# Optimization experiments

Measured on AMD Instinct MI355X. Metric: run time of the kernel, lower is better.

The kernel has to match this reference:

```python
import jax, jax.numpy as jnp
import numpy as np

D_MODEL = 1024
N_HEADS = 16
D_K = D_MODEL // N_HEADS
B, S = 2, 2048


def setup_inputs() -> dict:
    key = jax.random.key(0)
    ks = jax.random.split(key, 11)
    s = 1.0 / np.sqrt(D_MODEL)
    return {
        "q": jax.random.normal(ks[0], (B, S, D_MODEL), jnp.float32),
        "k": jax.random.normal(ks[1], (B, S, D_MODEL), jnp.float32),
        "v": jax.random.normal(ks[2], (B, S, D_MODEL), jnp.float32),
        "Wq": jax.random.normal(ks[3], (D_MODEL, D_MODEL), jnp.float32) * s,
        "bq": jnp.zeros((D_MODEL,), jnp.float32),
        "Wk": jax.random.normal(ks[4], (D_MODEL, D_MODEL), jnp.float32) * s,
        "bk": jnp.zeros((D_MODEL,), jnp.float32),
        "Wv": jax.random.normal(ks[5], (D_MODEL, D_MODEL), jnp.float32) * s,
        "bv": jnp.zeros((D_MODEL,), jnp.float32),
        "Wo": jax.random.normal(ks[6], (D_MODEL, D_MODEL), jnp.float32) * s,
        "bo": jnp.zeros((D_MODEL,), jnp.float32),
    }


def reference(q, k, v, Wq, bq, Wk, bk, Wv, bv, Wo, bo):
    b = q.shape[0]
    # linear projections then split heads: [b, s, d] -> [b, h, s, d_k]
    def proj(x, W, bias):
        y = jnp.einsum('bsd,ed->bse', x, W) + bias  # torch Linear: x @ W.T + b
        return y.reshape(b, -1, N_HEADS, D_K).transpose(0, 2, 1, 3)

    qh, kh, vh = proj(q, Wq, bq), proj(k, Wk, bk), proj(v, Wv, bv)
    scores = jnp.einsum('bhqd,bhkd->bhqk', qh, kh) / np.sqrt(D_K)
    attn = jax.nn.softmax(scores, axis=-1)  # dropout: identity (eval mode)
    x = jnp.einsum('bhqk,bhkd->bhqd', attn, vh)
    x = x.transpose(0, 2, 1, 3).reshape(b, -1, D_MODEL)
    return jnp.einsum('bsd,ed->bse', x, Wo) + bo
```

## Files before the change

kernel.cpp:

```cpp
#include <hip/hip_runtime.h>
#include <math.h>
#include <stdint.h>

#define DM 1024
#define NH 16
#define DKH 64
#define BB 2
#define SS 2048
#define MM (BB*SS)

typedef __bf16 bf16;
typedef __bf16 bf16x8 __attribute__((ext_vector_type(8)));
typedef float f32x4 __attribute__((ext_vector_type(4)));

#define MFMA16(a,b,c) __builtin_amdgcn_mfma_f32_16x16x32_bf16((a),(b),(c),0,0,0)

#define SOFTMAX_C 12.0f
#define QSCALE 0.1803368801111204f

__device__ static inline void g2l16(const void* g, void* l) {
  __builtin_amdgcn_global_load_lds(
      (const __attribute__((address_space(1))) unsigned int*)g,
      (__attribute__((address_space(3))) unsigned int*)l, 16, 0, 0);
}

__global__ __launch_bounds__(256) void cvt_all(
    const float* __restrict__ q, const float* __restrict__ k, const float* __restrict__ v,
    const float* __restrict__ wq, const float* __restrict__ wk,
    const float* __restrict__ wv, const float* __restrict__ wo,
    bf16* __restrict__ Xq, bf16* __restrict__ Xk, bf16* __restrict__ Xv,
    bf16* __restrict__ Wqb, bf16* __restrict__ Wkb, bf16* __restrict__ Wvb,
    bf16* __restrict__ Wob)
{
  const long i = (long)blockIdx.x * 256 + threadIdx.x;
  const float* src; bf16* dst; long off;
  if (i < 3L * 524288L) {
    const int a = (int)(i / 524288L);
    off = (i % 524288L) * 8;
    src = (a == 0) ? q : (a == 1) ? k : v;
    dst = (a == 0) ? Xq : (a == 1) ? Xk : Xv;
  } else {
    const long j = i - 3L * 524288L;
    const int a = (int)(j / 131072L);
    off = (j % 131072L) * 8;
    src = (a == 0) ? wq : (a == 1) ? wk : (a == 2) ? wv : wo;
    dst = (a == 0) ? Wqb : (a == 1) ? Wkb : (a == 2) ? Wvb : Wob;
  }
  float4 f0 = *(const float4*)(src + off);
  float4 f1 = *(const float4*)(src + off + 4);
  bf16x8 o;
  o[0] = (bf16)f0.x; o[1] = (bf16)f0.y; o[2] = (bf16)f0.z; o[3] = (bf16)f0.w;
  o[4] = (bf16)f1.x; o[5] = (bf16)f1.y; o[6] = (bf16)f1.z; o[7] = (bf16)f1.w;
  *(bf16x8*)(dst + off) = o;
}

template<int EP, int BN>
__device__ __forceinline__ void gemm_bt_body(
    const bf16* __restrict__ A, const bf16* __restrict__ W,
    const float* __restrict__ bias, void* __restrict__ Y, float scale)
{
  constexpr int NT = BN / 32;
  constexpr int PB = BN / 32;
  __shared__ __align__(16) char smem[16384 + BN * 128];
  const int tid = threadIdx.x;
  const int lane = tid & 63, w = tid >> 6;
  const int ln15 = lane & 15, q4 = lane >> 4;
  const int m0 = blockIdx.x * 128;
  const int n0 = blockIdx.y * BN;
  const int mhalf = (w >> 1) * 64, nhalf = (w & 1) * (BN / 2);

  const bf16* gA[4]; const bf16* gB[PB];
  char* lA[4]; char* lB[PB];
  #pragma unroll
  for (int p = 0; p < 4; ++p) {
    const int n = p * 256 + tid;
    const int row = n >> 3, u = n & 7;
    const int g = u ^ (row & 7);
    gA[p] = A + (size_t)(m0 + row) * DM + g * 8;
    lA[p] = smem + n * 16;
  }
  #pragma unroll
  for (int p = 0; p < PB; ++p) {
    const int n = p * 256 + tid;
    const int row = n >> 3, u = n & 7;
    const int g = u ^ (row & 7);
    gB[p] = W + (size_t)(n0 + row) * DM + g * 8;
    lB[p] = smem + 16384 + n * 16;
  }

  int aoff[4][2], boff[NT][2];
  #pragma unroll
  for (int mt = 0; mt < 4; ++mt) {
    const int row = mhalf + mt * 16 + ln15;
    #pragma unroll
    for (int kc = 0; kc < 2; ++kc)
      aoff[mt][kc] = (row * 8 + ((kc * 4 + q4) ^ (row & 7))) * 16;
  }
  #pragma unroll
  for (int nt = 0; nt < NT; ++nt) {
    const int row = nhalf + nt * 16 + ln15;
    #pragma unroll
    for (int kc = 0; kc < 2; ++kc)
      boff[nt][kc] = 16384 + (row * 8 + ((kc * 4 + q4) ^ (row & 7))) * 16;
  }

  f32x4 acc[4][NT] = {};

  for (int kt = 0; kt < DM; kt += 64) {
    __syncthreads();
    #pragma unroll
    for (int p = 0; p < 4; ++p) g2l16(gA[p] + kt, lA[p]);
    #pragma unroll
    for (int p = 0; p < PB; ++p) g2l16(gB[p] + kt, lB[p]);
    asm volatile("s_waitcnt vmcnt(0)" ::: "memory");
    __syncthreads();
    #pragma unroll
    for (int kc = 0; kc < 2; ++kc) {
      bf16x8 af[4];
      #pragma unroll
      for (int mt = 0; mt < 4; ++mt) af[mt] = *(const bf16x8*)(smem + aoff[mt][kc]);
      #pragma unroll
      for (int nt = 0; nt < NT; ++nt) {
        bf16x8 bfr = *(const bf16x8*)(smem + boff[nt][kc]);
        #pragma unroll
        for (int mt = 0; mt < 4; ++mt)
          acc[mt][nt] = MFMA16(af[mt], bfr, acc[mt][nt]);
      }
    }
  }

  #pragma unroll
  for (int nt = 0; nt < NT; ++nt) {
    const int col = n0 + nhalf + nt * 16 + ln15;
    const float bv = bias[col];
    #pragma unroll
    for (int mt = 0; mt < 4; ++mt) {
      #pragma unroll
      for (int r = 0; r < 4; ++r) {
        const int row = m0 + mhalf + mt * 16 + q4 * 4 + r;
        const float val = (acc[mt][nt][r] + bv) * scale;
        if (EP == 0) {
          ((float*)Y)[(size_t)row * DM + col] = val;
        } else {
          const int b = row >> 11, s = row & 2047;
          const int h = col >> 6, dk = col & 63;
          ((bf16*)Y)[(((size_t)(b * NH + h) * SS + s) * DKH) + dk] = (bf16)val;
        }
      }
    }
  }
}

__global__ __launch_bounds__(256) void gemm_qkv(
    const bf16* Xq, const bf16* Xk, const bf16* Xv,
    const bf16* Wq, const bf16* Wk, const bf16* Wv,
    const float* bq, const float* bk, const float* bv,
    bf16* qh, bf16* kh, bf16* vh)
{
  const int z = blockIdx.z;
  const bf16* A = (z == 0) ? Xq : (z == 1) ? Xk : Xv;
  const bf16* W = (z == 0) ? Wq : (z == 1) ? Wk : Wv;
  const float* bias = (z == 0) ? bq : (z == 1) ? bk : bv;
  bf16* Y = (z == 0) ? qh : (z == 1) ? kh : vh;
  const float scale = (z == 0) ? QSCALE : 1.0f;
  gemm_bt_body<1, 128>(A, W, bias, Y, scale);
}

__global__ __launch_bounds__(256) void gemm_out(
    const bf16* A, const bf16* W, const float* bias, float* Y)
{
  gemm_bt_body<0, 64>(A, W, bias, Y, 1.0f);
}

__global__ __launch_bounds__(256) void transpose_v(
    const bf16* __restrict__ vh, bf16* __restrict__ vth)
{
  __shared__ unsigned short Ls[64][66];
  const int bh = blockIdx.y;
  const int s0 = blockIdx.x * 64;
  const int tid = threadIdx.x;
  const unsigned short* src = (const unsigned short*)(vh + (size_t)bh * SS * DKH);
  unsigned short* dst = (unsigned short*)(vth + (size_t)bh * SS * DKH);
  #pragma unroll
  for (int p = 0; p < 2; ++p) {
    const int n = p * 256 + tid;
    const int sl = n >> 3, dc = (n & 7) * 8;
    uint4 a = *(const uint4*)(src + (size_t)(s0 + sl) * DKH + dc);
    Ls[sl][dc + 0] = (unsigned short)(a.x & 0xffff);
    Ls[sl][dc + 1] = (unsigned short)(a.x >> 16);
    Ls[sl][dc + 2] = (unsigned short)(a.y & 0xffff);
    Ls[sl][dc + 3] = (unsigned short)(a.y >> 16);
    Ls[sl][dc + 4] = (unsigned short)(a.z & 0xffff);
    Ls[sl][dc + 5] = (unsigned short)(a.z >> 16);
    Ls[sl][dc + 6] = (unsigned short)(a.w & 0xffff);
    Ls[sl][dc + 7] = (unsigned short)(a.w >> 16);
  }
  __syncthreads();
  #pragma unroll
  for (int p = 0; p < 2; ++p) {
    const int n = p * 256 + tid;
    const int dk = n >> 3, sc = (n & 7) * 8;
    uint4 o;
    o.x = (unsigned)Ls[sc + 0][dk] | ((unsigned)Ls[sc + 1][dk] << 16);
    o.y = (unsigned)Ls[sc + 2][dk] | ((unsigned)Ls[sc + 3][dk] << 16);
    o.z = (unsigned)Ls[sc + 4][dk] | ((unsigned)Ls[sc + 5][dk] << 16);
    o.w = (unsigned)Ls[sc + 6][dk] | ((unsigned)Ls[sc + 7][dk] << 16);
    *(uint4*)(dst + (size_t)dk * SS + s0 + sc) = o;
  }
}

__global__ __launch_bounds__(256) void attn_mfma(
    const bf16* __restrict__ Qh, const bf16* __restrict__ Kh,
    const bf16* __restrict__ Vth, bf16* __restrict__ Xout)
{
  __shared__ __align__(16) char smem[51200];
  const int tid = threadIdx.x, lane = tid & 63, w = tid >> 6;
  const int ln15 = lane & 15, q4 = lane >> 4;
  const int bh = blockIdx.y, b = bh >> 4, h = bh & 15;
  const int q0 = blockIdx.x * 128 + w * 32;
  const bf16* Qb = Qh + (size_t)bh * SS * DKH;
  const bf16* Kb = Kh + (size_t)bh * SS * DKH;
  const bf16* Vb = Vth + (size_t)bh * SS * DKH;

  bf16x8 qf[2][2];
  #pragma unroll
  for (int mt = 0; mt < 2; ++mt)
    #pragma unroll
    for (int kc = 0; kc < 2; ++kc)
      qf[mt][kc] = *(const bf16x8*)(Qb + (size_t)(q0 + mt * 16 + ln15) * DKH + kc * 32 + q4 * 8);

  bf16x8 ones_frag;
  {
    const bf16 o = (ln15 == 0) ? (bf16)1.0f : (bf16)0.0f;
    #pragma unroll
    for (int j = 0; j < 8; ++j) ones_frag[j] = o;
  }

  const bf16* gK[2]; const bf16* gV[2];
  char* lK[2]; char* lV[2];
  #pragma unroll
  for (int p = 0; p < 2; ++p) {
    const int n = p * 256 + tid;
    const int row = n >> 3, u = n & 7;
    const int g = u ^ (row & 7);
    gK[p] = Kb + (size_t)row * DKH + g * 8;
    gV[p] = Vb + (size_t)row * SS + g * 8;
    lK[p] = smem + n * 16;
    lV[p] = smem + 8192 + n * 16;
  }
  char* Pl = smem + 32768 + w * 4608;

  int koff[4][2], voff[4][2], poff[2][2];
  #pragma unroll
  for (int nt = 0; nt < 4; ++nt) {
    const int rowi = nt * 16 + ln15;
    #pragma unroll
    for (int kc = 0; kc < 2; ++kc) {
      koff[nt][kc] = (rowi * 8 + ((kc * 4 + q4) ^ (rowi & 7))) * 16;
      voff[nt][kc] = 8192 + (rowi * 8 + ((kc * 4 + q4) ^ (rowi & 7))) * 16;
    }
  }
  #pragma unroll
  for (int mt = 0; mt < 2; ++mt)
    #pragma unroll
    for (int kc = 0; kc < 2; ++kc)
      poff[mt][kc] = ((mt * 16 + ln15) * 9 + kc * 4 + q4) * 16;

  f32x4 Oa[2][4] = {};
  f32x4 Ol[2] = {};

  #pragma unroll
  for (int p = 0; p < 2; ++p) {
    g2l16(gK[p], lK[p]); g2l16(gV[p], lV[p]);
    gK[p] += 64 * DKH; gV[p] += 64;
  }

  for (int kt = 0; kt < SS / 64; ++kt) {
    const int cur = (kt & 1) << 14;
    asm volatile("s_waitcnt vmcnt(0)" ::: "memory");
    __syncthreads();
    if (kt < SS / 64 - 1) {
      const int nxt = (~kt & 1) << 14;
      #pragma unroll
      for (int p = 0; p < 2; ++p) {
        g2l16(gK[p], lK[p] + nxt); g2l16(gV[p], lV[p] + nxt);
        gK[p] += 64 * DKH; gV[p] += 64;
      }
    }

    f32x4 S[2][4];
    #pragma unroll
    for (int mt = 0; mt < 2; ++mt)
      #pragma unroll
      for (int nt = 0; nt < 4; ++nt)
        S[mt][nt] = (f32x4){-SOFTMAX_C, -SOFTMAX_C, -SOFTMAX_C, -SOFTMAX_C};
    #pragma unroll
    for (int kc = 0; kc < 2; ++kc) {
      #pragma unroll
      for (int nt = 0; nt < 4; ++nt) {
        bf16x8 kf = *(const bf16x8*)(smem + cur + koff[nt][kc]);
        #pragma unroll
        for (int mt = 0; mt < 2; ++mt)
          S[mt][nt] = MFMA16(qf[mt][kc], kf, S[mt][nt]);
      }
    }

    #pragma unroll
    for (int mt = 0; mt < 2; ++mt)
      #pragma unroll
      for (int nt = 0; nt < 4; ++nt)
        #pragma unroll
        for (int r = 0; r < 4; ++r) {
          const int prow = mt * 16 + q4 * 4 + r;
          const int key = nt * 16 + ln15;
          *(bf16*)(Pl + prow * 144 + key * 2) =
              (bf16)__builtin_amdgcn_exp2f(S[mt][nt][r]);
        }
    asm volatile("s_waitcnt lgkmcnt(0)" ::: "memory");

    #pragma unroll
    for (int kc = 0; kc < 2; ++kc) {
      bf16x8 pf[2];
      #pragma unroll
      for (int mt = 0; mt < 2; ++mt) pf[mt] = *(const bf16x8*)(Pl + poff[mt][kc]);
      #pragma unroll
      for (int nt = 0; nt < 4; ++nt) {
        bf16x8 vf = *(const bf16x8*)(smem + cur + voff[nt][kc]);
        #pragma unroll
        for (int mt = 0; mt < 2; ++mt)
          Oa[mt][nt] = MFMA16(pf[mt], vf, Oa[mt][nt]);
      }
      #pragma unroll
      for (int mt = 0; mt < 2; ++mt)
        Ol[mt] = MFMA16(pf[mt], ones_frag, Ol[mt]);
    }
  }

  #pragma unroll
  for (int mt = 0; mt < 2; ++mt)
    #pragma unroll
    for (int r = 0; r < 4; ++r) {
      const float l = __shfl(Ol[mt][r], lane & 48);
      const float inv = 1.f / l;
      const int srow = q0 + mt * 16 + q4 * 4 + r;
      #pragma unroll
      for (int nt = 0; nt < 4; ++nt) {
        const int col = h * DKH + nt * 16 + ln15;
        Xout[((size_t)(b * SS + srow)) * DM + col] = (bf16)(Oa[mt][nt][r] * inv);
      }
    }
}

extern "C" void kernel_launch(void* const* d_in, const int* in_sizes, int n_in,
                              void* d_out, int out_size, void* d_ws, size_t ws_size,
                              hipStream_t stream)
{
  const float* q  = (const float*)d_in[0];
  const float* k  = (const float*)d_in[1];
  const float* v  = (const float*)d_in[2];
  const float* Wq = (const float*)d_in[3];
  const float* bq = (const float*)d_in[4];
  const float* Wk = (const float*)d_in[5];
  const float* bk = (const float*)d_in[6];
  const float* Wv = (const float*)d_in[7];
  const float* bv = (const float*)d_in[8];
  const float* Wo = (const float*)d_in[9];
  const float* bo = (const float*)d_in[10];
  float* out = (float*)d_out;

  char* ws = (char*)d_ws;
  const size_t MB = 1u << 20;
  bf16* Xq  = (bf16*)(ws + 0);
  bf16* Xk  = (bf16*)(ws + 8 * MB);
  bf16* Xv  = (bf16*)(ws + 16 * MB);
  bf16* Wqb = (bf16*)(ws + 24 * MB);
  bf16* Wkb = (bf16*)(ws + 26 * MB);
  bf16* Wvb = (bf16*)(ws + 28 * MB);
  bf16* Wob = (bf16*)(ws + 30 * MB);
  bf16* qh  = (bf16*)(ws + 32 * MB);
  bf16* kh  = (bf16*)(ws + 40 * MB);
  bf16* vh  = (bf16*)(ws + 48 * MB);
  bf16* vth = (bf16*)(ws + 56 * MB);
  bf16* xh  = Xq;

  cvt_all<<<8192, 256, 0, stream>>>(q, k, v, Wq, Wk, Wv, Wo,
                                    Xq, Xk, Xv, Wqb, Wkb, Wvb, Wob);

  gemm_qkv<<<dim3(32, 8, 3), 256, 0, stream>>>(Xq, Xk, Xv, Wqb, Wkb, Wvb,
                                               bq, bk, bv, qh, kh, vh);

  transpose_v<<<dim3(32, 32), 256, 0, stream>>>(vh, vth);

  attn_mfma<<<dim3(16, 32), 256, 0, stream>>>(qh, kh, vth, xh);

  gemm_out<<<dim3(32, 16), 256, 0, stream>>>(xh, Wob, bo, out);
}
```

Baseline: 225.3 us.

## Keep attention probabilities in registers via transposed QK^T and K16 MFMA

Computes S transposed (K as the A operand) so each lane's exp'd scores already form the A-operand layout of a 16x16x16 bf16 MFMA. P can then feed the PV product directly from registers instead of round-tripping through LDS. The row sum moves from an extra MFMA against a ones fragment to register adds plus cross-lane shuffles. This cuts LDS use from 51200 to 32768 bytes, which may raise occupancy, and adjusts the V LDS offsets for 4-element fragments. The K16 MFMA issues twice as many instructions per unit of work as the K32 one.

```diff
diff --git a/kernel.cpp b/kernel.cpp
--- a/kernel.cpp
+++ b/kernel.cpp
@@ -11,9 +11,21 @@
 
 typedef __bf16 bf16;
 typedef __bf16 bf16x8 __attribute__((ext_vector_type(8)));
+typedef __bf16 bf16x4 __attribute__((ext_vector_type(4)));
+typedef short s16x4 __attribute__((ext_vector_type(4)));
 typedef float f32x4 __attribute__((ext_vector_type(4)));
 
 #define MFMA16(a,b,c) __builtin_amdgcn_mfma_f32_16x16x32_bf16((a),(b),(c),0,0,0)
+
+#if __has_builtin(__builtin_amdgcn_mfma_f32_16x16x16bf16_1k)
+#define MFMAK16(a,b,c) __builtin_amdgcn_mfma_f32_16x16x16bf16_1k((a),(b),(c),0,0,0)
+#else
+__device__ static inline f32x4 mfma_k16_asm(s16x4 a, s16x4 b, f32x4 c) {
+  asm("v_mfma_f32_16x16x16_bf16 %0, %1, %2, %0" : "+v"(c) : "v"(a), "v"(b));
+  return c;
+}
+#define MFMAK16(a,b,c) mfma_k16_asm((a),(b),(c))
+#endif
 
 #define SOFTMAX_C 12.0f
 #define QSCALE 0.1803368801111204f
@@ -213,7 +225,7 @@
     const bf16* __restrict__ Qh, const bf16* __restrict__ Kh,
     const bf16* __restrict__ Vth, bf16* __restrict__ Xout)
 {
-  __shared__ __align__(16) char smem[51200];
+  __shared__ __align__(16) char smem[32768];
   const int tid = threadIdx.x, lane = tid & 63, w = tid >> 6;
   const int ln15 = lane & 15, q4 = lane >> 4;
   const int bh = blockIdx.y, b = bh >> 4, h = bh & 15;
@@ -229,13 +241,6 @@
     for (int kc = 0; kc < 2; ++kc)
       qf[mt][kc] = *(const bf16x8*)(Qb + (size_t)(q0 + mt * 16 + ln15) * DKH + kc * 32 + q4 * 8);
 
-  bf16x8 ones_frag;
-  {
-    const bf16 o = (ln15 == 0) ? (bf16)1.0f : (bf16)0.0f;
-    #pragma unroll
-    for (int j = 0; j < 8; ++j) ones_frag[j] = o;
-  }
-
   const bf16* gK[2]; const bf16* gV[2];
   char* lK[2]; char* lV[2];
   #pragma unroll
@@ -248,26 +253,20 @@
     lK[p] = smem + n * 16;
     lV[p] = smem + 8192 + n * 16;
   }
-  char* Pl = smem + 32768 + w * 4608;
-
-  int koff[4][2], voff[4][2], poff[2][2];
-  #pragma unroll
-  for (int nt = 0; nt < 4; ++nt) {
-    const int rowi = nt * 16 + ln15;
-    #pragma unroll
-    for (int kc = 0; kc < 2; ++kc) {
-      koff[nt][kc] = (rowi * 8 + ((kc * 4 + q4) ^ (rowi & 7))) * 16;
-      voff[nt][kc] = 8192 + (rowi * 8 + ((kc * 4 + q4) ^ (rowi & 7))) * 16;
-    }
-  }
-  #pragma unroll
-  for (int mt = 0; mt < 2; ++mt)
-    #pragma unroll
-    for (int kc = 0; kc < 2; ++kc)
-      poff[mt][kc] = ((mt * 16 + ln15) * 9 + kc * 4 + q4) * 16;
+
+  int koff[2];
+  #pragma unroll
+  for (int kc = 0; kc < 2; ++kc)
+    koff[kc] = (ln15 * 8 + ((kc * 4 + q4) ^ (ln15 & 7))) * 16;
+  int voff[4];
+  #pragma unroll
+  for (int dt = 0; dt < 4; ++dt) {
+    const int row = dt * 16 + ln15;
+    voff[dt] = 8192 + row * 128 + (((q4 >> 1) ^ (row & 7)) * 16) + (q4 & 1) * 8;
+  }
 
   f32x4 Oa[2][4] = {};
-  f32x4 Ol[2] = {};
+  float lsum[2] = {0.f, 0.f};
 
   #pragma unroll
   for (int p = 0; p < 2; ++p) {
@@ -288,67 +287,68 @@
       }
     }
 
-    f32x4 S[2][4];
-    #pragma unroll
-    for (int mt = 0; mt < 2; ++mt)
-      #pragma unroll
-      for (int nt = 0; nt < 4; ++nt)
-        S[mt][nt] = (f32x4){-SOFTMAX_C, -SOFTMAX_C, -SOFTMAX_C, -SOFTMAX_C};
+    f32x4 S[4][2];
+    #pragma unroll
+    for (int nt = 0; nt < 4; ++nt)
+      #pragma unroll
+      for (int mt = 0; mt < 2; ++mt)
+        S[nt][mt] = (f32x4){-SOFTMAX_C, -SOFTMAX_C, -SOFTMAX_C, -SOFTMAX_C};
     #pragma unroll
     for (int kc = 0; kc < 2; ++kc) {
       #pragma unroll
       for (int nt = 0; nt < 4; ++nt) {
-        bf16x8 kf = *(const bf16x8*)(smem + cur + koff[nt][kc]);
+        const bf16x8 kf = *(const bf16x8*)(smem + cur + koff[kc] + nt * 2048);
         #pragma unroll
         for (int mt = 0; mt < 2; ++mt)
-          S[mt][nt] = MFMA16(qf[mt][kc], kf, S[mt][nt]);
-      }
-    }
-
-    #pragma unroll
-    for (int mt = 0; mt < 2; ++mt)
-      #pragma unroll
-      for (int nt = 0; nt < 4; ++nt)
-        #pragma unroll
-        for (int r = 0; r < 4; ++r) {
-          const int prow = mt * 16 + q4 * 4 + r;
-          const int key = nt * 16 + ln15;
-          *(bf16*)(Pl + prow * 144 + key * 2) =
-              (bf16)__builtin_amdgcn_exp2f(S[mt][nt][r]);
-        }
-    asm volatile("s_waitcnt lgkmcnt(0)" ::: "memory");
-
-    #pragma unroll
-    for (int kc = 0; kc < 2; ++kc) {
-      bf16x8 pf[2];
-      #pragma unroll
-      for (int mt = 0; mt < 2; ++mt) pf[mt] = *(const bf16x8*)(Pl + poff[mt][kc]);
+          S[nt][mt] = MFMA16(kf, qf[mt][kc], S[nt][mt]);
+      }
+    }
+
+    s16x4 pf[2][4];
+    #pragma unroll
+    for (int mt = 0; mt < 2; ++mt) {
       #pragma unroll
       for (int nt = 0; nt < 4; ++nt) {
-        bf16x8 vf = *(const bf16x8*)(smem + cur + voff[nt][kc]);
+        const float p0 = __builtin_amdgcn_exp2f(S[nt][mt][0]);
+        const float p1 = __builtin_amdgcn_exp2f(S[nt][mt][1]);
+        const float p2 = __builtin_amdgcn_exp2f(S[nt][mt][2]);
+        const float p3 = __builtin_amdgcn_exp2f(S[nt][mt][3]);
+        lsum[mt] += (p0 + p1) + (p2 + p3);
+        union { bf16x4 b; s16x4 s; } u;
+        u.b[0] = (bf16)p0; u.b[1] = (bf16)p1; u.b[2] = (bf16)p2; u.b[3] = (bf16)p3;
+        pf[mt][nt] = u.s;
+      }
+    }
+
+    #pragma unroll
+    for (int nt = 0; nt < 4; ++nt) {
+      #pragma unroll
+      for (int dt = 0; dt < 4; ++dt) {
+        const s16x4 vf = *(const s16x4*)(smem + cur + (voff[dt] ^ (nt << 5)));
         #pragma unroll
         for (int mt = 0; mt < 2; ++mt)
-          Oa[mt][nt] = MFMA16(pf[mt], vf, Oa[mt][nt]);
-      }
-      #pragma unroll
-      for (int mt = 0; mt < 2; ++mt)
-        Ol[mt] = MFMA16(pf[mt], ones_frag, Ol[mt]);
-    }
-  }
-
-  #pragma unroll
-  for (int mt = 0; mt < 2; ++mt)
+          Oa[mt][dt] = MFMAK16(pf[mt][nt], vf, Oa[mt][dt]);
+      }
+    }
+  }
+
+  #pragma unroll
+  for (int mt = 0; mt < 2; ++mt) {
+    float l = lsum[mt];
+    l += __shfl_xor(l, 16);
+    l += __shfl_xor(l, 32);
     #pragma unroll
     for (int r = 0; r < 4; ++r) {
-      const float l = __shfl(Ol[mt][r], lane & 48);
-      const float inv = 1.f / l;
+      const float lr = __shfl(l, (q4 << 2) | r);
+      const float inv = 1.f / lr;
       const int srow = q0 + mt * 16 + q4 * 4 + r;
       #pragma unroll
-      for (int nt = 0; nt < 4; ++nt) {
-        const int col = h * DKH + nt * 16 + ln15;
-        Xout[((size_t)(b * SS + srow)) * DM + col] = (bf16)(Oa[mt][nt][r] * inv);
-      }
-    }
+      for (int dt = 0; dt < 4; ++dt) {
+        const int col = h * DKH + dt * 16 + ln15;
+        Xout[((size_t)(b * SS + srow)) * DM + col] = (bf16)(Oa[mt][dt][r] * inv);
+      }
+    }
+  }
 }
 
 extern "C" void kernel_launch(void* const* d_in, const int* in_sizes, int n_in,
```

New measurement: 217.3 us. 1.04x faster.
